# Kernel optimization log

Hardware: AMD Instinct MI355X
Metric: run time of the kernel (lower is better)

The kernel has to match this reference:

```python
import jax, jax.numpy as jnp
import numpy as np

B, C, H, W = 2, 64, 192, 192
C8 = C // 8


def setup_inputs() -> dict:
    key = jax.random.key(0)
    ks = jax.random.split(key, 8)
    return {
        "x": jax.random.normal(ks[0], (B, C, H, W), jnp.float32),
        "Wq": jax.random.normal(ks[1], (C8, C), jnp.float32) * 0.05,
        "bq": jax.random.normal(ks[2], (C8,), jnp.float32) * 0.05,
        "Wk": jax.random.normal(ks[3], (C8, C), jnp.float32) * 0.05,
        "bk": jax.random.normal(ks[4], (C8,), jnp.float32) * 0.05,
        "Wv": jax.random.normal(ks[5], (C, C), jnp.float32) * 0.05,
        "bv": jax.random.normal(ks[6], (C,), jnp.float32) * 0.05,
        "gamma": jax.random.normal(ks[7], (1,), jnp.float32),
    }


def _offsets(t):
    # [B, Cc, H, W] -> [B, 16, Cc, L]; per chessboard offset (i,j) in the 4x4
    # block, value = max(t[.., 4h+i, 4w+j], 0)  (mask-then-maxpool in the original)
    b, cc, h, w = t.shape
    hq, wq = h // 4, w // 4
    r = t.reshape(b, cc, hq, 4, wq, 4)
    r = jnp.transpose(r, (0, 3, 5, 1, 2, 4)).reshape(b, 16, cc, hq * wq)
    return jnp.maximum(r, 0.0)


def reference(x, Wq, bq, Wk, bk, Wv, bv, gamma):
    b, c, h, w = x.shape
    hq, wq = h // 4, w // 4
    q = jnp.einsum('oc,bchw->bohw', Wq, x) + bq[None, :, None, None]
    k = jnp.einsum('oc,bchw->bohw', Wk, x) + bk[None, :, None, None]
    v = jnp.einsum('oc,bchw->bohw', Wv, x) + bv[None, :, None, None]
    qs = _offsets(q)  # [B,16,C8,L]
    ks = _offsets(k)  # [B,16,C8,L]
    vs = _offsets(v)  # [B,16,C,L]
    # attn[b,n,l,m] = softmax_m( q_l . k_m )
    attn = jax.nn.softmax(jnp.einsum('bncl,bncm->bnlm', qs, ks), axis=-1)
    out = jnp.einsum('bncm,bnlm->bncl', vs, attn)  # [B,16,C,L]
    # scatter each offset's [C,Hq,Wq] result back to its chessboard position
    out = out.reshape(b, 4, 4, c, hq, wq)
    out = jnp.transpose(out, (0, 3, 4, 1, 5, 2)).reshape(b, c, h, w)
    return gamma[0] * out + x
```

## Files before the change

### kernel.cpp

```cpp
#include <hip/hip_runtime.h>

#define LOG2E 1.44269504088896340736f

constexpr int C_ = 64, H_ = 192, W_ = 192;
constexpr int WQ_ = 48, L_ = 2304;
constexpr int KVB = 64;
constexpr int NMT = L_ / KVB;
constexpr int QROWS = 32;
constexpr int NQT = L_ / QROWS;
constexpr int NBLK = 32 * NQT;
constexpr int WROW = 96;
constexpr int NCOL = 18432;
constexpr int PBLK = (NCOL / 64) * 4;

typedef _Float16 half8  __attribute__((ext_vector_type(8)));
typedef short    bf16x8 __attribute__((ext_vector_type(8)));
typedef float    f32x16 __attribute__((ext_vector_type(16)));
typedef uint     u32x2  __attribute__((ext_vector_type(2)));
typedef uint     u32x4  __attribute__((ext_vector_type(4)));

static __device__ inline f32x16 fzero16() {
    f32x16 v;
    #pragma unroll
    for (int i = 0; i < 16; ++i) v[i] = 0.f;
    return v;
}

static __device__ inline uint cvtpk_bf16(float lo, float hi) {
    uint r;
    asm("v_cvt_pk_bf16_f32 %0, %1, %2" : "=v"(r) : "v"(lo), "v"(hi));
    return r;
}

static __device__ inline ushort f2bf(float f) {
    uint u = __builtin_bit_cast(uint, f);
    u = (u + 0x7FFFu + ((u >> 16) & 1u)) >> 16;
    return (ushort)u;
}

__global__ __launch_bounds__(256) void wtrans_kernel(
    const float* __restrict__ Wq, const float* __restrict__ bq,
    const float* __restrict__ Wk, const float* __restrict__ bk,
    const float* __restrict__ Wv, const float* __restrict__ bv,
    float* __restrict__ wT)
{
    for (int idx = threadIdx.x; idx < 64 * WROW; idx += 256) {
        const int c = idx / WROW, j = idx - c * WROW;
        float v = 0.f;
        if (j < 64)      v = Wv[j * 64 + c];
        else if (j < 72) v = LOG2E * Wq[(j - 64) * 64 + c];
        else if (j < 80) v = Wk[(j - 72) * 64 + c];
        wT[idx] = v;
    }
    for (int i = threadIdx.x; i < WROW; i += 256) {
        float v = 0.f;
        if (i < 64)      v = bv[i];
        else if (i < 72) v = LOG2E * bq[i - 64];
        else if (i < 80) v = bk[i - 72];
        wT[64 * WROW + i] = v;
    }
}

__global__ __launch_bounds__(64) void proj_kernel(
    const float* __restrict__ x, const float* __restrict__ wT,
    _Float16* __restrict__ qh, _Float16* __restrict__ kh,
    ushort* __restrict__ vws)
{
    const int bid0 = blockIdx.x;
    const int bid = (bid0 & 7) * (PBLK / 8) + (bid0 >> 3);
    const int cg = bid >> 2;
    const int j  = bid & 3;
    const int lane = threadIdx.x;
    const int C = cg * 64 + lane;
    const int b = C / 9216;
    const int cp = C - b * 9216;
    const int h = cp / 48;
    const int wq = cp - h * 48;
    const int n = (h & 3) * 4 + j;
    const int l = (h >> 2) * 48 + wq;
    const int bn = b * 16 + n;

    const float* xp = x + (size_t)b * 64 * 36864 + cp * 4 + j;

    float acc[20] = {};
    #pragma unroll 4
    for (int c = 0; c < 64; ++c) {
        const float xv = xp[(size_t)c * 36864];
        const float4* w4 = (const float4*)(wT + c * WROW + j * 20);
        #pragma unroll
        for (int jj = 0; jj < 5; ++jj) {
            const float4 wv = w4[jj];
            acc[4 * jj + 0] += wv.x * xv;
            acc[4 * jj + 1] += wv.y * xv;
            acc[4 * jj + 2] += wv.z * xv;
            acc[4 * jj + 3] += wv.w * xv;
        }
    }

    const float* bias = wT + 64 * WROW;
    const int mt = l >> 6;
    const int ks4 = (l >> 4) & 3;
    const int m16 = l & 15;
    ushort* vd = vws + (((size_t)bn * NMT + mt) * 4 + ks4) * 1024 + m16;

    if (j < 3) {
        #pragma unroll
        for (int o = 0; o < 20; ++o)
            vd[(20 * j + o) * 16] = f2bf(fmaxf(acc[o] + bias[20 * j + o], 0.f));
    } else {
        #pragma unroll
        for (int o = 0; o < 4; ++o)
            vd[(60 + o) * 16] = f2bf(fmaxf(acc[o] + bias[60 + o], 0.f));
        half8 qv, kv;
        #pragma unroll
        for (int o = 0; o < 8; ++o) {
            qv[o] = (_Float16)fmaxf(acc[4 + o] + bias[64 + o], 0.f);
            kv[o] = (_Float16)fmaxf(acc[12 + o] + bias[72 + o], 0.f);
        }
        *(half8*)(qh + ((size_t)bn * L_ + l) * 8) = qv;
        *(half8*)(kh + ((size_t)bn * L_ + l) * 8) = kv;
    }
}

__global__ __launch_bounds__(256) void attn_kernel(
    const _Float16* __restrict__ qh, const _Float16* __restrict__ kh,
    const ushort* __restrict__ vws, const float* __restrict__ x,
    const float* __restrict__ gamma_p, float* __restrict__ out)
{
    __shared__ float red[4][64][17];
    float* lds_o = &red[0][0][0];

    const int tid = threadIdx.x;
    const int wid = tid >> 6;
    const int lane = tid & 63;
    const int r32 = lane & 31;
    const int hi = lane >> 5;

    const int bid0 = blockIdx.x;
    const int bid = (bid0 & 7) * (NBLK / 8) + (bid0 >> 3);
    const int bn = bid / NQT;
    const int lt = bid - bn * NQT;
    const int b = bn >> 4, n = bn & 15;
    const int qrow0 = lt * QROWS;

    const _Float16* qb = qh + (size_t)bn * L_ * 8;
    const _Float16* kb = kh + (size_t)bn * L_ * 8;
    const ushort* vaddr = vws + (size_t)bn * NMT * 4096 + r32 * 16 + hi * 8;

    half8 qfrag;
    #pragma unroll
    for (int i = 0; i < 8; ++i) qfrag[i] = (_Float16)0.f;
    if (hi == 0) qfrag = *(const half8*)(qb + (qrow0 + r32) * 8);

    f32x16 acc0 = fzero16(), acc1 = fzero16();
    float psum = 0.f;

    half8 kf0n, kf1n;
    #pragma unroll
    for (int i = 0; i < 8; ++i) { kf0n[i] = (_Float16)0.f; kf1n[i] = (_Float16)0.f; }

    if (hi == 0) {
        kf0n = *(const half8*)(kb + (wid * 64 + r32) * 8);
        kf1n = *(const half8*)(kb + (wid * 64 + 32 + r32) * 8);
    }
    f32x16 s0 = __builtin_amdgcn_mfma_f32_32x32x16_f16(kf0n, qfrag, fzero16(), 0, 0, 0);
    f32x16 s1 = __builtin_amdgcn_mfma_f32_32x32x16_f16(kf1n, qfrag, fzero16(), 0, 0, 0);

    bf16x8 vb0[4], vb1[4];
    vb0[0] = *(const bf16x8*)(vaddr + wid * 4096);
    vb1[0] = *(const bf16x8*)(vaddr + wid * 4096 + 512);
    vb0[1] = *(const bf16x8*)(vaddr + wid * 4096 + 1024);
    vb1[1] = *(const bf16x8*)(vaddr + wid * 4096 + 1024 + 512);
    vb0[2] = *(const bf16x8*)(vaddr + wid * 4096 + 2048);
    vb1[2] = *(const bf16x8*)(vaddr + wid * 4096 + 2048 + 512);

    #pragma unroll 1
    for (int t = 0; t < NMT / 4; ++t) {
        const int mt  = 4 * t + wid;
        const int mtn = (t < NMT / 4 - 1) ? mt + 4 : mt;

        if (hi == 0) {
            kf0n = *(const half8*)(kb + (mtn * 64 + r32) * 8);
            kf1n = *(const half8*)(kb + (mtn * 64 + 32 + r32) * 8);
        }

        #define STAGE(KS, SV, HALF, LS, LOFF)                                  \
        {                                                                      \
            const bf16x8 nv0 = *(const bf16x8*)(vaddr + (LOFF));               \
            const bf16x8 nv1 = *(const bf16x8*)(vaddr + (LOFF) + 512);         \
            float e[8];                                                        \
            _Pragma("unroll")                                                  \
            for (int i = 0; i < 8; ++i)                                        \
                e[i] = __builtin_amdgcn_exp2f(SV[(HALF) * 8 + i]);             \
            psum += ((e[0] + e[1]) + (e[2] + e[3]))                            \
                  + ((e[4] + e[5]) + (e[6] + e[7]));                           \
            const uint pb0 = cvtpk_bf16(e[0], e[1]);                           \
            const uint pb1 = cvtpk_bf16(e[2], e[3]);                           \
            const uint pa0 = cvtpk_bf16(e[4], e[5]);                           \
            const uint pa1 = cvtpk_bf16(e[6], e[7]);                           \
            const u32x2 q0 = __builtin_amdgcn_permlane32_swap(pa0, pb0, false, false); \
            const u32x2 q1 = __builtin_amdgcn_permlane32_swap(pa1, pb1, false, false); \
            u32x4 tt;                                                          \
            tt[0] = q0.y; tt[1] = q1.y; tt[2] = q0.x; tt[3] = q1.x;            \
            const bf16x8 pa = __builtin_bit_cast(bf16x8, tt);                  \
            __builtin_amdgcn_s_setprio(1);                                     \
            acc0 = __builtin_amdgcn_mfma_f32_32x32x16_bf16(pa, vb0[KS], acc0, 0, 0, 0); \
            acc1 = __builtin_amdgcn_mfma_f32_32x32x16_bf16(pa, vb1[KS], acc1, 0, 0, 0); \
            __builtin_amdgcn_s_setprio(0);                                     \
            vb0[LS] = nv0; vb1[LS] = nv1;                                      \
        }

        STAGE(0, s0, 0, 3, mt * 4096 + 3072)
        STAGE(1, s0, 1, 0, mtn * 4096)
        s0 = __builtin_amdgcn_mfma_f32_32x32x16_f16(kf0n, qfrag, fzero16(), 0, 0, 0);
        STAGE(2, s1, 0, 1, mtn * 4096 + 1024)
        STAGE(3, s1, 1, 2, mtn * 4096 + 2048)
        s1 = __builtin_amdgcn_mfma_f32_32x32x16_f16(kf1n, qfrag, fzero16(), 0, 0, 0);
        #undef STAGE
    }

    const uint pu = __builtin_bit_cast(uint, psum);
    const u32x2 pc = __builtin_amdgcn_permlane32_swap(pu, pu, false, false);
    const float other = __builtin_bit_cast(float, (hi == 0) ? pc.x : pc.y);
    const float wsum = psum + other;

    {
        float* dst = &red[wid][lane][0];
        #pragma unroll
        for (int r = 0; r < 16; ++r) dst[r] = acc0[r];
        dst[16] = wsum;
    }
    __syncthreads();

    float rtot = 0.f;
    #pragma unroll
    for (int w4 = 0; w4 < 4; ++w4) rtot += red[w4][lane][16];
    const float rinv = 1.0f / rtot;

    const int sw = wid & 1;
    float fin[8];
    if (wid < 2) {
        #pragma unroll
        for (int i = 0; i < 8; ++i)
            fin[i] = red[0][lane][8 * sw + i] + red[1][lane][8 * sw + i]
                   + red[2][lane][8 * sw + i] + red[3][lane][8 * sw + i];
    }
    __syncthreads();

    {
        float* dst = &red[wid][lane][0];
        #pragma unroll
        for (int r = 0; r < 16; ++r) dst[r] = acc1[r];
    }
    __syncthreads();

    if (wid >= 2) {
        #pragma unroll
        for (int i = 0; i < 8; ++i)
            fin[i] = red[0][lane][8 * sw + i] + red[1][lane][8 * sw + i]
                   + red[2][lane][8 * sw + i] + red[3][lane][8 * sw + i];
    }
    __syncthreads();

    {
        const int chw = r32 + ((wid >= 2) ? 32 : 0);
        #pragma unroll
        for (int i = 0; i < 8; ++i) {
            const int r = 8 * sw + i;
            const int Rg = (r & 3) + 8 * (r >> 2) + 4 * hi;
            const float ri = __shfl(rinv, Rg, 64);
            lds_o[chw * 33 + Rg] = fin[i] * ri;
        }
    }
    __syncthreads();

    const int gl = lane & 31;
    const int ch2 = lane >> 5;
    const int glf = qrow0 + gl;
    const int hh = (glf / WQ_) * 4 + (n >> 2);
    const int ww = (glf % WQ_) * 4 + (n & 3);
    const float g = gamma_p[0];
    const size_t base = ((size_t)b * C_ * H_ + hh) * W_ + ww;
    #pragma unroll
    for (int io = 0; io < 8; ++io) {
        const int ch = io * 8 + wid * 2 + ch2;
        const size_t o = base + (size_t)ch * (H_ * W_);
        out[o] = g * lds_o[ch * 33 + gl] + x[o];
    }
}

extern "C" void kernel_launch(void* const* d_in, const int* in_sizes, int n_in,
                              void* d_out, int out_size, void* d_ws, size_t ws_size,
                              hipStream_t stream) {
    const float* x  = (const float*)d_in[0];
    const float* Wq = (const float*)d_in[1];
    const float* bq = (const float*)d_in[2];
    const float* Wk = (const float*)d_in[3];
    const float* bk = (const float*)d_in[4];
    const float* Wv = (const float*)d_in[5];
    const float* bv = (const float*)d_in[6];
    const float* gamma = (const float*)d_in[7];
    float* out = (float*)d_out;

    float* wT = (float*)d_ws;
    _Float16* qh = (_Float16*)(wT + 8192);
    _Float16* kh = qh + (size_t)32 * L_ * 8;
    ushort*   vb = (ushort*)(kh + (size_t)32 * L_ * 8);

    wtrans_kernel<<<dim3(1), dim3(256), 0, stream>>>(Wq, bq, Wk, bk, Wv, bv, wT);
    proj_kernel<<<dim3(PBLK), dim3(64), 0, stream>>>(x, wT, qh, kh, vb);
    attn_kernel<<<dim3(NBLK), dim3(256), 0, stream>>>(qh, kh, vb, x, gamma, out);
}
```

Before: 77.11 us.

## Compute softmax row sums via MFMA with ones vector and prefetch residual x

Replaces the per-lane scalar accumulation of exponentials with a third bf16 MFMA against an all-ones B operand, so the row sums come out of the matrix unit and are reduced through a small shared buffer. It also loads the residual x values at kernel start, hiding their latency behind the attention loop. The aim is to drop VALU adds from the hot loop. The cost is one extra MFMA per stage, extra accumulator registers, and row sums taken from the bf16-rounded probabilities rather than fp32 values.

```diff
diff --git a/kernel.cpp b/kernel.cpp
--- a/kernel.cpp
+++ b/kernel.cpp
@@ -128,6 +128,7 @@
     const float* __restrict__ gamma_p, float* __restrict__ out)
 {
     __shared__ float red[4][64][17];
+    __shared__ float red_s[4][2][16];
     float* lds_o = &red[0][0][0];
 
     const int tid = threadIdx.x;
@@ -147,13 +148,29 @@
     const _Float16* kb = kh + (size_t)bn * L_ * 8;
     const ushort* vaddr = vws + (size_t)bn * NMT * 4096 + r32 * 16 + hi * 8;
 
+    const int egl = lane & 31;
+    const int ech2 = lane >> 5;
+    const int eglf = qrow0 + egl;
+    const int ehh = (eglf / WQ_) * 4 + (n >> 2);
+    const int eww = (eglf % WQ_) * 4 + (n & 3);
+    const size_t ebase = ((size_t)b * C_ * H_ + ehh) * W_ + eww;
+    float xpre[8];
+    #pragma unroll
+    for (int io = 0; io < 8; ++io) {
+        const int ch = io * 8 + wid * 2 + ech2;
+        xpre[io] = x[ebase + (size_t)ch * (H_ * W_)];
+    }
+
     half8 qfrag;
     #pragma unroll
     for (int i = 0; i < 8; ++i) qfrag[i] = (_Float16)0.f;
     if (hi == 0) qfrag = *(const half8*)(qb + (qrow0 + r32) * 8);
 
-    f32x16 acc0 = fzero16(), acc1 = fzero16();
-    float psum = 0.f;
+    bf16x8 vones;
+    #pragma unroll
+    for (int i = 0; i < 8; ++i) vones[i] = (short)0x3F80;
+
+    f32x16 acc0 = fzero16(), acc1 = fzero16(), acc_s = fzero16();
 
     half8 kf0n, kf1n;
     #pragma unroll
@@ -192,8 +209,6 @@
             _Pragma("unroll")                                                  \
             for (int i = 0; i < 8; ++i)                                        \
                 e[i] = __builtin_amdgcn_exp2f(SV[(HALF) * 8 + i]);             \
-            psum += ((e[0] + e[1]) + (e[2] + e[3]))                            \
-                  + ((e[4] + e[5]) + (e[6] + e[7]));                           \
             const uint pb0 = cvtpk_bf16(e[0], e[1]);                           \
             const uint pb1 = cvtpk_bf16(e[2], e[3]);                           \
             const uint pa0 = cvtpk_bf16(e[4], e[5]);                           \
@@ -206,6 +221,7 @@
             __builtin_amdgcn_s_setprio(1);                                     \
             acc0 = __builtin_amdgcn_mfma_f32_32x32x16_bf16(pa, vb0[KS], acc0, 0, 0, 0); \
             acc1 = __builtin_amdgcn_mfma_f32_32x32x16_bf16(pa, vb1[KS], acc1, 0, 0, 0); \
+            acc_s = __builtin_amdgcn_mfma_f32_32x32x16_bf16(pa, vones, acc_s, 0, 0, 0); \
             __builtin_amdgcn_s_setprio(0);                                     \
             vb0[LS] = nv0; vb1[LS] = nv1;                                      \
         }
@@ -219,22 +235,22 @@
         #undef STAGE
     }
 
-    const uint pu = __builtin_bit_cast(uint, psum);
-    const u32x2 pc = __builtin_amdgcn_permlane32_swap(pu, pu, false, false);
-    const float other = __builtin_bit_cast(float, (hi == 0) ? pc.x : pc.y);
-    const float wsum = psum + other;
-
     {
         float* dst = &red[wid][lane][0];
         #pragma unroll
         for (int r = 0; r < 16; ++r) dst[r] = acc0[r];
-        dst[16] = wsum;
-    }
-    __syncthreads();
-
-    float rtot = 0.f;
-    #pragma unroll
-    for (int w4 = 0; w4 < 4; ++w4) rtot += red[w4][lane][16];
+        if (r32 == 0) {
+            #pragma unroll
+            for (int r = 0; r < 16; ++r) red_s[wid][hi][r] = acc_s[r];
+        }
+    }
+    __syncthreads();
+
+    const int q  = lane & 31;
+    const int hq = (q >> 2) & 1;
+    const int rq = (q & 3) | ((q >> 3) << 2);
+    const float rtot = red_s[0][hq][rq] + red_s[1][hq][rq]
+                     + red_s[2][hq][rq] + red_s[3][hq][rq];
     const float rinv = 1.0f / rtot;
 
     const int sw = wid & 1;
@@ -274,18 +290,12 @@
     }
     __syncthreads();
 
-    const int gl = lane & 31;
-    const int ch2 = lane >> 5;
-    const int glf = qrow0 + gl;
-    const int hh = (glf / WQ_) * 4 + (n >> 2);
-    const int ww = (glf % WQ_) * 4 + (n & 3);
     const float g = gamma_p[0];
-    const size_t base = ((size_t)b * C_ * H_ + hh) * W_ + ww;
     #pragma unroll
     for (int io = 0; io < 8; ++io) {
-        const int ch = io * 8 + wid * 2 + ch2;
-        const size_t o = base + (size_t)ch * (H_ * W_);
-        out[o] = g * lds_o[ch * 33 + gl] + x[o];
+        const int ch = io * 8 + wid * 2 + ech2;
+        const size_t o = ebase + (size_t)ch * (H_ * W_);
+        out[o] = g * lds_o[ch * 33 + egl] + xpre[io];
     }
 }
 
```

Result: slower. 81.46 us (+5.6%).
